# Optimization experiments

Hardware: AMD Instinct MI355X
Metric: run time of the kernel (lower is better)

Reference implementation:

```python
import jax, jax.numpy as jnp
import numpy as np


def setup_inputs() -> dict:
    key = jax.random.key(0)
    k1, k2, k3, k4, k5 = jax.random.split(key, 5)
    B, S, IN, OUT, G = 8, 2048, 4096, 4096, 32
    NB = OUT * IN // G  # 524288 blocks
    x = jax.random.normal(k1, (B, S, IN), dtype=jnp.float32)
    # two int4 values packed per byte -> G//2 bytes per block
    weight_packed = jax.random.randint(k2, (NB, G // 2), 0, 256, dtype=jnp.int32)
    weight_scale = (jax.random.uniform(k3, (NB, 1)) * 0.02).astype(jnp.float16)
    weight_var_mask = jax.random.randint(k4, (NB,), 0, 2) > 0
    bias = jax.random.normal(k5, (OUT,), dtype=jnp.float32)
    return {"x": x, "weight_packed": weight_packed, "weight_scale": weight_scale,
            "weight_var_mask": weight_var_mask, "bias": bias}


def _block_dequantize_mixed(packed, scale, mask):
    # packed: [NB, G//2] int32 holding two uint4 per byte
    # scale:  [NB, 1] fp16 per-block scale; mask: [NB] bool (high-variance blocks keep full scale)
    q_lo = packed & 0xF
    q_hi = (packed >> 4) & 0xF
    q = jnp.stack([q_lo, q_hi], axis=-1).reshape(packed.shape[0], -1)  # [NB, G], interleaved
    scale_eff = scale.astype(jnp.float32) * jnp.where(mask[:, None], 1.0, 0.5)
    return (q.astype(jnp.float32) - 8.0) * scale_eff  # [NB, G]


def reference(x, weight_packed, weight_scale, weight_var_mask, bias):
    out_features = bias.shape[0]
    in_features = x.shape[-1]
    w = _block_dequantize_mixed(weight_packed, weight_scale, weight_var_mask)
    w = w.reshape(out_features, in_features)  # [OUT, IN]
    # y = x @ w^T + b
    return jnp.einsum('bsi,oi->bso', x, w) + bias
```

## Files before the change

kernel.cpp:

```cpp
#include <hip/hip_runtime.h>
#include <hip/hip_bf16.h>
#include <stdint.h>

#define M_TOT 16384
#define N_TOT 4096
#define K_TOT 4096
#define NB    524288

#define BM 256
#define BN 256
#define BK 64
#define NT (K_TOT / BK)

typedef __attribute__((ext_vector_type(8))) __bf16 bf16x8;
typedef __attribute__((ext_vector_type(4))) float f32x4;

#define BARF() do { asm volatile("" ::: "memory"); \
                    __builtin_amdgcn_s_barrier(); \
                    asm volatile("" ::: "memory"); } while (0)
#define VMW(n) asm volatile("s_waitcnt vmcnt(" #n ")" ::: "memory")

#define MFMA1(d, a, b) d = __builtin_amdgcn_mfma_f32_16x16x32_bf16(a, b, d, 0, 0, 0)
#define MFMA_PAIR(mb, A0, A1) do { \
  _Pragma("unroll") \
  for (int j_ = 0; j_ < 4; ++j_) { \
    MFMA1(acc[mb][j_],     A0[0], bF[j_][0]); \
    MFMA1(acc[mb][j_],     A0[1], bF[j_][1]); \
    MFMA1(acc[(mb)+1][j_], A1[0], bF[j_][0]); \
    MFMA1(acc[(mb)+1][j_], A1[1], bF[j_][1]); \
  } \
} while (0)

__global__ __launch_bounds__(256) void dequant_w(
    const int* __restrict__ packed,
    const float* __restrict__ scale,
    const int* __restrict__ mask,
    __hip_bfloat16* __restrict__ wout)
{
    int t = blockIdx.x * blockDim.x + threadIdx.x;
    const int4 pk = ((const int4*)packed)[t];
    int nb = t >> 2;
    float se = scale[nb] * (mask[nb] ? 1.0f : 0.5f);
    int vals[4] = { pk.x, pk.y, pk.z, pk.w };
    __hip_bfloat16 o[8];
#pragma unroll
    for (int j = 0; j < 4; ++j) {
        int v = vals[j];
        o[2*j]   = __float2bfloat16((float)((v & 0xF) - 8) * se);
        o[2*j+1] = __float2bfloat16((float)(((v >> 4) & 0xF) - 8) * se);
    }
    int4 st;
    __builtin_memcpy(&st, o, 16);
    ((int4*)wout)[t] = st;
}

__global__ __launch_bounds__(256) void cvt_x(
    const float* __restrict__ x, __hip_bfloat16* __restrict__ xb)
{
    int t = blockIdx.x * blockDim.x + threadIdx.x;
    const float4* xp = (const float4*)x;
    float4 a = xp[2*t], b = xp[2*t + 1];
    __hip_bfloat16 o[8] = {
        __float2bfloat16(a.x), __float2bfloat16(a.y),
        __float2bfloat16(a.z), __float2bfloat16(a.w),
        __float2bfloat16(b.x), __float2bfloat16(b.y),
        __float2bfloat16(b.z), __float2bfloat16(b.w)
    };
    int4 st;
    __builtin_memcpy(&st, o, 16);
    ((int4*)xb)[t] = st;
}

__global__ __launch_bounds__(512, 2) void gemm_bt(
    const __hip_bfloat16* __restrict__ A,
    const __hip_bfloat16* __restrict__ Bw,
    const float* __restrict__ bias,
    float* __restrict__ C)
{
    __shared__ __align__(16) char lds[131072];

    const int tid  = threadIdx.x;
    const int lane = tid & 63;
    const int wave = tid >> 6;
    const int wm = wave >> 2;
    const int wn = wave & 3;

    const int wg = (blockIdx.x & 7) * 128 + (blockIdx.x >> 3);
    const int mt = wg & 63;
    const int nt = wg >> 6;
    const int m0 = mt * BM;
    const int n0 = nt * BN;

    const int srow = tid >> 3;
    const int scb  = ((tid & 7) * 16) ^ (((tid >> 3) & 7) << 4);
    const char* gA = (const char*)A  + ((size_t)(m0 + srow) * K_TOT) * 2 + scb;
    const char* gB = (const char*)Bw + ((size_t)(n0 + srow) * K_TOT) * 2 + scb;
    char* lA = (char*)lds + tid * 16;
    char* lB = (char*)lds + 32768 + tid * 16;

    auto stA = [&](int t, int h) {
        if (t >= NT) t -= 2;
        const int p = t & 1;
        const size_t kb = (size_t)t * (BK * 2);
#pragma unroll
        for (int s = 0; s < 2; ++s) {
            const int r = 2 * h + s;
            __builtin_amdgcn_global_load_lds(
                (const __attribute__((address_space(1))) void*)
                    (gA + kb + (size_t)r * 64 * K_TOT * 2),
                (__attribute__((address_space(3))) void*)
                    (lA + p * 65536 + r * 8192), 16, 0, 0);
        }
    };
    auto stB = [&](int t, int h) {
        if (t >= NT) t -= 2;
        const int p = t & 1;
        const size_t kb = (size_t)t * (BK * 2);
#pragma unroll
        for (int s = 0; s < 2; ++s) {
            const int r = 2 * h + s;
            __builtin_amdgcn_global_load_lds(
                (const __attribute__((address_space(1))) void*)
                    (gB + kb + (size_t)r * 64 * K_TOT * 2),
                (__attribute__((address_space(3))) void*)
                    (lB + p * 65536 + r * 8192), 16, 0, 0);
        }
    };

    const int swz  = (lane & 7) << 4;
    const int pcb0 = (((lane >> 4) * 16) + 0)  ^ swz;
    const int pcb1 = (((lane >> 4) * 16) + 64) ^ swz;
    int arow[8], brow[4];
#pragma unroll
    for (int i = 0; i < 8; ++i) arow[i] = (wm * 128 + i * 16 + (lane & 15)) * 128;
#pragma unroll
    for (int j = 0; j < 4; ++j) brow[j] = (wn * 64 + j * 16 + (lane & 15)) * 128;

    f32x4 acc[8][4] = {};

    const char* ldsA0 = (const char*)lds;
    const char* ldsB0 = (const char*)lds + 32768;
    const char* ldsA1 = (const char*)lds + 65536;
    const char* ldsB1 = (const char*)lds + 98304;

#define TILE_BLOCK(Ap, Bp, STG1, STG2, STG3, STG4) do { \
    bf16x8 bF[4][2]; bf16x8 a67[2][2]; \
    {  \
        bf16x8 a01[2][2]; \
        _Pragma("unroll") \
        for (int j_ = 0; j_ < 4; ++j_) { \
            bF[j_][0] = *(const bf16x8*)((Bp) + brow[j_] + pcb0); \
            bF[j_][1] = *(const bf16x8*)((Bp) + brow[j_] + pcb1); \
        } \
        _Pragma("unroll") \
        for (int m_ = 0; m_ < 2; ++m_) { \
            a01[m_][0] = *(const bf16x8*)((Ap) + arow[m_] + pcb0); \
            a01[m_][1] = *(const bf16x8*)((Ap) + arow[m_] + pcb1); \
        } \
        STG1; \
        BARF(); \
        __builtin_amdgcn_s_setprio(1); \
        MFMA_PAIR(0, a01[0], a01[1]); \
        __builtin_amdgcn_s_setprio(0); \
        BARF(); \
    } \
    {  \
        bf16x8 a23[2][2]; \
        _Pragma("unroll") \
        for (int m_ = 0; m_ < 2; ++m_) { \
            a23[m_][0] = *(const bf16x8*)((Ap) + arow[2 + m_] + pcb0); \
            a23[m_][1] = *(const bf16x8*)((Ap) + arow[2 + m_] + pcb1); \
        } \
        STG2; \
        BARF(); \
        __builtin_amdgcn_s_setprio(1); \
        MFMA_PAIR(2, a23[0], a23[1]); \
        __builtin_amdgcn_s_setprio(0); \
        BARF(); \
    } \
    {  \
        bf16x8 a45[2][2]; \
        _Pragma("unroll") \
        for (int m_ = 0; m_ < 2; ++m_) { \
            a45[m_][0] = *(const bf16x8*)((Ap) + arow[4 + m_] + pcb0); \
            a45[m_][1] = *(const bf16x8*)((Ap) + arow[4 + m_] + pcb1); \
            a67[m_][0] = *(const bf16x8*)((Ap) + arow[6 + m_] + pcb0); \
            a67[m_][1] = *(const bf16x8*)((Ap) + arow[6 + m_] + pcb1); \
        } \
        STG3; \
        BARF(); \
        __builtin_amdgcn_s_setprio(1); \
        MFMA_PAIR(4, a45[0], a45[1]); \
        __builtin_amdgcn_s_setprio(0); \
        BARF(); \
    } \
    {  \
        STG4; \
        BARF(); \
        __builtin_amdgcn_s_setprio(1); \
        MFMA_PAIR(6, a67[0], a67[1]); \
        __builtin_amdgcn_s_setprio(0); \
        VMW(6); \
        BARF(); \
    } \
} while (0)

    stB(0, 0); stB(0, 1); stA(0, 0); stA(0, 1);
    stB(1, 0); stB(1, 1); stA(1, 0);
    VMW(6);
    BARF();

    for (int it = 0; it < NT / 2; ++it) {
        const int ta = 2 * it, tb = ta + 1;
        TILE_BLOCK(ldsA0, ldsB0,
                   stA(tb, 1), stB(ta + 2, 0), stB(ta + 2, 1), stA(ta + 2, 0));
        TILE_BLOCK(ldsA1, ldsB1,
                   stA(ta + 2, 1), stB(tb + 2, 0), stB(tb + 2, 1), stA(tb + 2, 0));
    }
#undef TILE_BLOCK

    VMW(0);
    BARF();

    const int cl = lane & 15;
    const int rq = (lane >> 4) * 4;
#pragma unroll
    for (int j = 0; j < 4; ++j) {
        const int col = n0 + wn * 64 + j * 16 + cl;
        const float bv = bias[col];
#pragma unroll
        for (int i = 0; i < 8; ++i) {
            const size_t rbase = (size_t)(m0 + wm * 128 + i * 16 + rq);
#pragma unroll
            for (int r = 0; r < 4; ++r) {
                C[(rbase + r) * N_TOT + col] = acc[i][j][r] + bv;
            }
        }
    }
}

extern "C" void kernel_launch(void* const* d_in, const int* in_sizes, int n_in,
                              void* d_out, int out_size, void* d_ws, size_t ws_size,
                              hipStream_t stream) {
    const float* x      = (const float*)d_in[0];
    const int*   wp     = (const int*)d_in[1];
    const float* wscale = (const float*)d_in[2];
    const int*   wmask  = (const int*)d_in[3];
    const float* bias   = (const float*)d_in[4];
    float*       out    = (float*)d_out;

    __hip_bfloat16* Wb = (__hip_bfloat16*)d_ws;
    __hip_bfloat16* Xb = (__hip_bfloat16*)((char*)d_ws + (size_t)N_TOT * K_TOT * 2);

    dequant_w<<<(NB * 4) / 256, 256, 0, stream>>>(wp, wscale, wmask, Wb);
    cvt_x<<<((size_t)M_TOT * K_TOT / 8) / 256, 256, 0, stream>>>(x, Xb);
    gemm_bt<<<(M_TOT / BM) * (N_TOT / BN), 512, 0, stream>>>(Xb, Wb, bias, out);
}
```

Measured before the change: 903.4 us.

## Restructure GEMM main loop into three-phase pipeline with double-buffered A fragments

Reorganizes the GEMM k-loop schedule: each 64-wide k-tile now issues all four A-tile global-to-LDS loads at once, followed by the two B-half loads, instead of four interleaved stages. A fragments are ping-ponged between two register sets (aCur/aNxt), so LDS reads for the next MFMA group overlap with current MFMAs. This removes the pre-MFMA barrier in each sub-phase, cutting barriers per tile from eight to four. The wait count changes to vmcnt(4) and the final drain moves after the epilogue; this changes how far prefetches stay in flight and risks LDS read/write hazards if the ordering is off.

```diff
diff --git a/kernel.cpp b/kernel.cpp
--- a/kernel.cpp
+++ b/kernel.cpp
@@ -98,13 +98,12 @@
     char* lA = (char*)lds + tid * 16;
     char* lB = (char*)lds + 32768 + tid * 16;
 
-    auto stA = [&](int t, int h) {
+    auto stA4 = [&](int t) {
         if (t >= NT) t -= 2;
         const int p = t & 1;
         const size_t kb = (size_t)t * (BK * 2);
 #pragma unroll
-        for (int s = 0; s < 2; ++s) {
-            const int r = 2 * h + s;
+        for (int r = 0; r < 4; ++r) {
             __builtin_amdgcn_global_load_lds(
                 (const __attribute__((address_space(1))) void*)
                     (gA + kb + (size_t)r * 64 * K_TOT * 2),
@@ -112,7 +111,7 @@
                     (lA + p * 65536 + r * 8192), 16, 0, 0);
         }
     };
-    auto stB = [&](int t, int h) {
+    auto stB2 = [&](int t, int h) {
         if (t >= NT) t -= 2;
         const int p = t & 1;
         const size_t kb = (size_t)t * (BK * 2);
@@ -143,84 +142,62 @@
     const char* ldsA1 = (const char*)lds + 65536;
     const char* ldsB1 = (const char*)lds + 98304;
 
-#define TILE_BLOCK(Ap, Bp, STG1, STG2, STG3, STG4) do { \
-    bf16x8 bF[4][2]; bf16x8 a67[2][2]; \
-    {  \
-        bf16x8 a01[2][2]; \
-        _Pragma("unroll") \
-        for (int j_ = 0; j_ < 4; ++j_) { \
-            bF[j_][0] = *(const bf16x8*)((Bp) + brow[j_] + pcb0); \
-            bF[j_][1] = *(const bf16x8*)((Bp) + brow[j_] + pcb1); \
-        } \
-        _Pragma("unroll") \
-        for (int m_ = 0; m_ < 2; ++m_) { \
-            a01[m_][0] = *(const bf16x8*)((Ap) + arow[m_] + pcb0); \
-            a01[m_][1] = *(const bf16x8*)((Ap) + arow[m_] + pcb1); \
-        } \
-        STG1; \
-        BARF(); \
-        __builtin_amdgcn_s_setprio(1); \
-        MFMA_PAIR(0, a01[0], a01[1]); \
-        __builtin_amdgcn_s_setprio(0); \
-        BARF(); \
-    } \
-    {  \
-        bf16x8 a23[2][2]; \
-        _Pragma("unroll") \
-        for (int m_ = 0; m_ < 2; ++m_) { \
-            a23[m_][0] = *(const bf16x8*)((Ap) + arow[2 + m_] + pcb0); \
-            a23[m_][1] = *(const bf16x8*)((Ap) + arow[2 + m_] + pcb1); \
-        } \
-        STG2; \
-        BARF(); \
-        __builtin_amdgcn_s_setprio(1); \
-        MFMA_PAIR(2, a23[0], a23[1]); \
-        __builtin_amdgcn_s_setprio(0); \
-        BARF(); \
-    } \
-    {  \
-        bf16x8 a45[2][2]; \
-        _Pragma("unroll") \
-        for (int m_ = 0; m_ < 2; ++m_) { \
-            a45[m_][0] = *(const bf16x8*)((Ap) + arow[4 + m_] + pcb0); \
-            a45[m_][1] = *(const bf16x8*)((Ap) + arow[4 + m_] + pcb1); \
-            a67[m_][0] = *(const bf16x8*)((Ap) + arow[6 + m_] + pcb0); \
-            a67[m_][1] = *(const bf16x8*)((Ap) + arow[6 + m_] + pcb1); \
-        } \
-        STG3; \
-        BARF(); \
-        __builtin_amdgcn_s_setprio(1); \
-        MFMA_PAIR(4, a45[0], a45[1]); \
-        __builtin_amdgcn_s_setprio(0); \
-        BARF(); \
-    } \
-    {  \
-        STG4; \
-        BARF(); \
-        __builtin_amdgcn_s_setprio(1); \
-        MFMA_PAIR(6, a67[0], a67[1]); \
-        __builtin_amdgcn_s_setprio(0); \
-        VMW(6); \
-        BARF(); \
-    } \
+#define TILE_BLOCK(Ap, Bp, STG_A, STG_B0, STG_B1) do { \
+    bf16x8 bF[4][2], aCur[2][2], aNxt[2][2]; \
+     \
+    _Pragma("unroll") \
+    for (int j_ = 0; j_ < 4; ++j_) { \
+        bF[j_][0] = *(const bf16x8*)((Bp) + brow[j_] + pcb0); \
+        bF[j_][1] = *(const bf16x8*)((Bp) + brow[j_] + pcb1); \
+    } \
+    _Pragma("unroll") \
+    for (int m_ = 0; m_ < 2; ++m_) { \
+        aCur[m_][0] = *(const bf16x8*)((Ap) + arow[m_] + pcb0); \
+        aCur[m_][1] = *(const bf16x8*)((Ap) + arow[m_] + pcb1); \
+        aNxt[m_][0] = *(const bf16x8*)((Ap) + arow[2 + m_] + pcb0); \
+        aNxt[m_][1] = *(const bf16x8*)((Ap) + arow[2 + m_] + pcb1); \
+    } \
+    STG_A; \
+    __builtin_amdgcn_s_setprio(1); MFMA_PAIR(0, aCur[0], aCur[1]); \
+    __builtin_amdgcn_s_setprio(0); \
+    BARF(); \
+     \
+    _Pragma("unroll") \
+    for (int m_ = 0; m_ < 2; ++m_) { \
+        aCur[m_][0] = *(const bf16x8*)((Ap) + arow[4 + m_] + pcb0); \
+        aCur[m_][1] = *(const bf16x8*)((Ap) + arow[4 + m_] + pcb1); \
+    } \
+    STG_B0; \
+    __builtin_amdgcn_s_setprio(1); MFMA_PAIR(2, aNxt[0], aNxt[1]); \
+    __builtin_amdgcn_s_setprio(0); \
+    BARF(); \
+     \
+    _Pragma("unroll") \
+    for (int m_ = 0; m_ < 2; ++m_) { \
+        aNxt[m_][0] = *(const bf16x8*)((Ap) + arow[6 + m_] + pcb0); \
+        aNxt[m_][1] = *(const bf16x8*)((Ap) + arow[6 + m_] + pcb1); \
+    } \
+    STG_B1; \
+    __builtin_amdgcn_s_setprio(1); MFMA_PAIR(4, aCur[0], aCur[1]); \
+    __builtin_amdgcn_s_setprio(0); \
+    BARF(); \
+     \
+    __builtin_amdgcn_s_setprio(1); MFMA_PAIR(6, aNxt[0], aNxt[1]); \
+    __builtin_amdgcn_s_setprio(0); \
+    VMW(4); \
+    BARF(); \
 } while (0)
 
-    stB(0, 0); stB(0, 1); stA(0, 0); stA(0, 1);
-    stB(1, 0); stB(1, 1); stA(1, 0);
-    VMW(6);
+    stB2(0, 0); stB2(0, 1); stA4(0); stB2(1, 0); stB2(1, 1);
+    VMW(4);
     BARF();
 
     for (int it = 0; it < NT / 2; ++it) {
         const int ta = 2 * it, tb = ta + 1;
-        TILE_BLOCK(ldsA0, ldsB0,
-                   stA(tb, 1), stB(ta + 2, 0), stB(ta + 2, 1), stA(ta + 2, 0));
-        TILE_BLOCK(ldsA1, ldsB1,
-                   stA(ta + 2, 1), stB(tb + 2, 0), stB(tb + 2, 1), stA(tb + 2, 0));
+        TILE_BLOCK(ldsA0, ldsB0, stA4(tb),     stB2(ta + 2, 0), stB2(ta + 2, 1));
+        TILE_BLOCK(ldsA1, ldsB1, stA4(ta + 2), stB2(tb + 2, 0), stB2(tb + 2, 1));
     }
 #undef TILE_BLOCK
-
-    VMW(0);
-    BARF();
 
     const int cl = lane & 15;
     const int rq = (lane >> 4) * 4;
@@ -237,6 +214,7 @@
             }
         }
     }
+    VMW(0);
 }
 
 extern "C" void kernel_launch(void* const* d_in, const int* in_sizes, int n_in,
```

New measurement: 897.0 us. Within noise of the previous version (-0.7%).
